# Kernel tuning notes

Measured on AMD Instinct MI355X. Metric: run time of the kernel, lower is better.

## Reference

```python
import jax, jax.numpy as jnp
from jax import lax
import numpy as np

B = 32768
N_IN = 8
N_HID = 64
N_CTRL = 2
M_SCEN = (1.0, 1.2)          # scenario parameters for f/g
M_NOM = 1.0
CLF_LAM = 1.0
CBF_LAM = 1.0
P_CLF = 100.0
P_CBF = 50.0
QP_ITERS = 80                # fixed-iteration batched ADMM (OSQP-style) replacing CvxpyLayer
RHO = 1.0
SIGMA = 1e-6
INF = jnp.inf


def setup_inputs() -> dict:
    key = jax.random.key(0)
    ks = jax.random.split(key, 16)
    s = 0.3
    return {
        "x":   jax.random.normal(ks[0], (B, N_IN), jnp.float32),
        "VW1": jax.random.normal(ks[1], (N_HID, N_IN), jnp.float32) * s,
        "Vb1": jax.random.normal(ks[2], (N_HID,), jnp.float32) * s,
        "VW2": jax.random.normal(ks[3], (N_HID, N_HID), jnp.float32) * s,
        "Vb2": jax.random.normal(ks[4], (N_HID,), jnp.float32) * s,
        "HW1": jax.random.normal(ks[5], (N_HID, N_IN), jnp.float32) * s,
        "Hb1": jax.random.normal(ks[6], (N_HID,), jnp.float32) * s,
        "HW2": jax.random.normal(ks[7], (N_HID, N_HID), jnp.float32) * s,
        "Hb2": jax.random.normal(ks[8], (N_HID,), jnp.float32) * s,
        "HW3": jax.random.normal(ks[9], (N_HID, N_HID), jnp.float32) * s,
        "Hb3": jax.random.normal(ks[10], (N_HID,), jnp.float32) * s,
        "HW4": jax.random.normal(ks[11], (1, N_HID), jnp.float32) * s,
        "Hb4": jax.random.normal(ks[12], (1,), jnp.float32) * s,
        "G0":  jax.random.normal(ks[13], (N_IN, N_CTRL), jnp.float32) * s,
        "K":   jax.random.normal(ks[14], (N_IN, N_CTRL), jnp.float32) * s,
    }


def _lyapunov(x, W1, b1, W2, b2):
    t1 = jnp.tanh(x @ W1.T + b1)                                   # [B,H]
    t2 = jnp.tanh(t1 @ W2.T + b2)                                  # [B,H]
    V = 0.5 * jnp.sum(t2 * t2, axis=1)                             # [B]
    # fused diag(1-t^2) @ W chain (no diag_embed materialization)
    D1 = (1.0 - t1 ** 2)[:, :, None] * W1[None]                    # [B,H,N]
    D2 = (1.0 - t2 ** 2)[:, :, None] * jnp.einsum('hk,bkn->bhn', W2, D1)
    grad_V = jnp.einsum('bh,bhn->bn', t2, D2)                      # [B,N]
    return V, grad_V


def _barrier(x, W1, b1, W2, b2, W3, b3, W4, b4):
    t1 = jnp.tanh(x @ W1.T + b1)
    t2 = jnp.tanh(t1 @ W2.T + b2)
    t3 = jnp.tanh(t2 @ W3.T + b3)
    H = t3 @ W4.T + b4                                             # [B,1]
    D1 = (1.0 - t1 ** 2)[:, :, None] * W1[None]
    D2 = (1.0 - t2 ** 2)[:, :, None] * jnp.einsum('hk,bkn->bhn', W2, D1)
    D3 = (1.0 - t3 ** 2)[:, :, None] * jnp.einsum('hk,bkn->bhn', W3, D2)
    grad_H = jnp.einsum('oh,bhn->bn', W4, D3)                      # [B,N] (o=1)
    return H, grad_H


def _solve_qp(q, A, lo, hi):
    """Batched OSQP-style ADMM for min 0.5 z^T P z + q^T z  s.t. lo <= A z <= hi.
    P = diag([2,2,0,0,0,0]); z = [u(2), r_clf(2), s_cbf(2)]. Fixed iterations."""
    nb, mc, nz = A.shape[0], A.shape[1], A.shape[2]
    Pdiag = jnp.array([2.0, 2.0, 0.0, 0.0, 0.0, 0.0], q.dtype)
    M = RHO * jnp.einsum('bmi,bmj->bij', A, A) + jnp.diag(Pdiag + SIGMA)
    Minv = jnp.linalg.inv(M)                                       # [B,6,6]
    x0 = jnp.zeros((nb, nz), q.dtype)
    z0 = jnp.zeros((nb, mc), q.dtype)
    y0 = jnp.zeros((nb, mc), q.dtype)

    def step(carry, _):
        xx, zz, yy = carry
        rhs = SIGMA * xx - q + jnp.einsum('bmi,bm->bi', A, RHO * zz - yy)
        xt = jnp.einsum('bij,bj->bi', Minv, rhs)
        zt = jnp.einsum('bmi,bi->bm', A, xt)
        zn = jnp.clip(zt + yy / RHO, lo, hi)
        yn = yy + RHO * (zt - zn)
        return (xt, zn, yn), None

    (xf, _, _), _ = lax.scan(step, (x0, z0, y0), None, length=QP_ITERS)
    return xf                                                      # [B,6]


def _forward(x, VW1, Vb1, VW2, Vb2, HW1, Hb1, HW2, Hb2, HW3, Hb3, HW4, Hb4, G0, K):
    V, grad_V = _lyapunov(x, VW1, Vb1, VW2, Vb2)
    H, grad_H = _barrier(x, HW1, Hb1, HW2, Hb2, HW3, Hb3, HW4, Hb4)

    LfVs, LgVs, LfHs, LgHs = [], [], [], []
    for m in M_SCEN:
        # f(x,m) = -x/m ; g(x,m) = G0/m
        LfVs.append(-jnp.sum(grad_V * x, axis=1) / m)              # [B]
        LgVs.append((grad_V @ G0) / m)                             # [B,C]
        LfHs.append(-jnp.sum(grad_H * x, axis=1) / m)
        LgHs.append((grad_H @ G0) / m)
    u_nom = -(x @ K) * (1.0 / M_NOM)                               # [B,C]

    nb = x.shape[0]
    z2 = jnp.zeros((nb, 2), x.dtype)
    ey = jnp.eye(2, dtype=x.dtype)
    e = lambda i: jnp.broadcast_to(ey[i], (nb, 2))
    ninf = jnp.full((nb,), -INF, x.dtype)
    pinf = jnp.full((nb,), INF, x.dtype)
    zer = jnp.zeros((nb,), x.dtype)

    rows, los, his = [], [], []
    for i in range(len(M_SCEN)):
        # CBF: LfH + LgH@u + cbf_lam*H + s_i >= 0
        rows.append(jnp.concatenate([LgHs[i], z2, e(i)], axis=1))
        los.append(-(LfHs[i] + CBF_LAM * H[:, 0])); his.append(pinf)
        # CLF: LfV + LgV@u + clf_lam*V - r_i <= 0
        rows.append(jnp.concatenate([LgVs[i], -e(i), z2], axis=1))
        los.append(ninf); his.append(-(LfVs[i] + CLF_LAM * V))
    for i in range(len(M_SCEN)):
        rows.append(jnp.concatenate([z2, e(i), z2], axis=1)); los.append(zer); his.append(pinf)
    for i in range(len(M_SCEN)):
        rows.append(jnp.concatenate([z2, z2, e(i)], axis=1)); los.append(zer); his.append(pinf)

    A = jnp.stack(rows, axis=1)                                    # [B,8,6]
    lo = jnp.stack(los, axis=1)                                    # [B,8]
    hi = jnp.stack(his, axis=1)
    # objective ||u-u_nom||^2 + p_clf*sum r + p_cbf*sum s  ->  q = [-2 u_nom, p_clf, p_clf, p_cbf, p_cbf]
    q = jnp.concatenate([-2.0 * u_nom,
                         jnp.full((nb, 2), P_CLF, x.dtype),
                         jnp.full((nb, 2), P_CBF, x.dtype)], axis=1)

    z = _solve_qp(q, A, lo, hi)                                    # [B,6]
    u = z[:, :N_CTRL]
    relaxation = jnp.mean(z[:, N_CTRL:N_CTRL + len(M_SCEN)], axis=1, keepdims=True)  # [B,1]

    ns = float(len(M_SCEN))
    Vdot = sum(LfVs[i] + jnp.sum(LgVs[i] * u, axis=1) for i in range(len(M_SCEN))) / ns
    Hdot = sum(LfHs[i] + jnp.sum(LgHs[i] * u, axis=1) for i in range(len(M_SCEN))) / ns
    return u, relaxation, V, Vdot[:, None, None], H, Hdot[:, None, None]


def reference(x, VW1, Vb1, VW2, Vb2, HW1, Hb1, HW2, Hb2, HW3, Hb3, HW4, Hb4, G0, K):
    return _forward(x, VW1, Vb1, VW2, Vb2, HW1, Hb1, HW2, Hb2, HW3, Hb3, HW4, Hb4, G0, K)
```

## Files before the change

kernel.cpp:

```cpp
#include <hip/hip_runtime.h>
#include <hip/hip_bf16.h>
#include <math.h>

typedef _Float16 f16x8 __attribute__((ext_vector_type(8)));
typedef _Float16 f16x4 __attribute__((ext_vector_type(4)));
typedef float    f32x4 __attribute__((ext_vector_type(4)));

__device__ __forceinline__ float ldin(const void* p, int i, int f32f) {
  return f32f ? ((const float*)p)[i]
              : __bfloat162float(((const __hip_bfloat16*)p)[i]);
}

__device__ __forceinline__ f32x4 MFMA(f16x8 a, f16x8 b, f32x4 c) {
  return __builtin_amdgcn_mfma_f32_16x16x32_f16(a, b, c, 0, 0, 0);
}

__device__ __forceinline__ float tanh_fast(float x) {
  float e = __expf(2.f * x);
  return 1.f - 2.f * __builtin_amdgcn_rcpf(e + 1.f);
}

__device__ __forceinline__ float redq(float v) {
  v += __shfl_xor(v, 16, 64);
  v += __shfl_xor(v, 32, 64);
  return v;
}

__device__ __forceinline__ int widx(int h, int k) {
  return ((h >> 4) << 10) + ((k >> 5) << 9) + (((k >> 3) & 3) << 7) + ((h & 15) << 3) + (k & 7);
}

#define OFF_W2V   0
#define OFF_W2VT  4096
#define OFF_W2H   8192
#define OFF_W2HT  12288
#define OFF_W3H   16384
#define OFF_W3HT  20480
#define OFF_W1V   24576
#define OFF_W1H   26624
#define SW_N      28672

#define C_WGV0 0
#define C_WGV1 64
#define C_WGH0 128
#define C_WGH1 192
#define C_VB1  256
#define C_VB2  320
#define C_HB1  384
#define C_HB2  448
#define C_HB3  512
#define C_W4   576
#define C_K    640
#define C_HB4  656
#define C_N    660

__global__ __launch_bounds__(512, 2) void fused_kernel(
    const void* px, const void* pVW1, const void* pVb1, const void* pVW2, const void* pVb2,
    const void* pHW1, const void* pHb1, const void* pHW2, const void* pHb2,
    const void* pHW3, const void* pHb3, const void* pHW4, const void* pHb4,
    const void* pG0, const void* pK, float* out)
{
  __shared__ __align__(16) _Float16 sW[SW_N];
  __shared__ __align__(16) _Float16 sAct[16][1024];
  __shared__ __align__(16) float sQPs[128][12];
  __shared__ __align__(16) float sC[C_N];
  __shared__ int sCnt;

  const int tid = threadIdx.x;
  if (tid == 0) sCnt = 0;
  __syncthreads();
  {
    const unsigned short* xbp = (const unsigned short*)px;
    int good = 0;
#pragma unroll
    for (int i = 0; i < 2; ++i) {
      int ex = (xbp[tid * 2 + i] >> 7) & 0xFF;
      good += (ex >= 97 && ex <= 157) ? 1 : 0;
    }
    atomicAdd(&sCnt, good);
  }
  __syncthreads();
  const int f32f = (sCnt >= 870) ? 0 : 1;

  {
    const int h = tid >> 3, k0 = (tid & 7) * 8;
    auto prepM = [&](const void* src, int offF, int offT) {
      f16x8 vv;
#pragma unroll
      for (int j = 0; j < 8; ++j) vv[j] = (_Float16)ldin(src, tid * 8 + j, f32f);
      *(f16x8*)(sW + offF + widx(h, k0)) = vv;
#pragma unroll
      for (int j = 0; j < 8; ++j) sW[offT + widx(k0 + j, h)] = vv[j];
    };
    prepM(pVW2, OFF_W2V, OFF_W2VT);
    prepM(pHW2, OFF_W2H, OFF_W2HT);
    prepM(pHW3, OFF_W3H, OFF_W3HT);

    if (tid < 64) {
      const int ht = tid >> 4, mm = tid & 15;
      auto prepW1 = [&](const void* src, int off) {
        const int base = off + ht * 512 + mm * 8;
#pragma unroll
        for (int j = 0; j < 8; ++j) {
          float wv = ldin(src, tid * 8 + j, f32f);
          _Float16 hh = (_Float16)wv;
          sW[base + j]       = hh;
          sW[base + 128 + j] = hh;
          sW[base + 256 + j] = f32f ? (_Float16)(wv - (float)hh)
                                    : (_Float16)0.f;
          sW[base + 384 + j] = (_Float16)0.f;
        }
      };
      prepW1(pVW1, OFF_W1V);
      prepW1(pHW1, OFF_W1H);
      float a0 = 0.f, a1 = 0.f, b0 = 0.f, b1 = 0.f;
#pragma unroll
      for (int nn = 0; nn < 8; ++nn) {
        float g0 = ldin(pG0, 2 * nn, f32f), g1 = ldin(pG0, 2 * nn + 1, f32f);
        float wv = ldin(pVW1, tid * 8 + nn, f32f), wh = ldin(pHW1, tid * 8 + nn, f32f);
        a0 += wv * g0; a1 += wv * g1; b0 += wh * g0; b1 += wh * g1;
      }
      sC[C_WGV0 + tid] = a0; sC[C_WGV1 + tid] = a1;
      sC[C_WGH0 + tid] = b0; sC[C_WGH1 + tid] = b1;
      sC[C_VB1 + tid] = ldin(pVb1, tid, f32f);
      sC[C_VB2 + tid] = ldin(pVb2, tid, f32f);
      sC[C_HB1 + tid] = ldin(pHb1, tid, f32f);
      sC[C_HB2 + tid] = ldin(pHb2, tid, f32f);
      sC[C_HB3 + tid] = ldin(pHb3, tid, f32f);
      sC[C_W4  + tid] = ldin(pHW4, tid, f32f);
    }
    if (tid < 16) sC[C_K + tid] = ldin(pK, tid, f32f);
    if (tid == 0) sC[C_HB4] = ldin(pHb4, 0, f32f);
  }
  __syncthreads();

  const int lane = tid & 63, w = tid >> 6;
  const int n = lane & 15, q = lane >> 4;
  const int e0 = blockIdx.x * 128 + w * 16;

  float un0 = 0.f, un1 = 0.f;
  f16x8 xb;
#pragma unroll
  for (int j = 0; j < 8; ++j) {
    float xv = ldin(px, (e0 + n) * 8 + j, f32f);
    _Float16 hh = (_Float16)xv;
    float lo = xv - (float)hh;
    xb[j] = (q == 1) ? (_Float16)lo : ((q == 3) ? (_Float16)0.f : hh);
    un0 -= xv * sC[C_K + 2 * j];
    un1 -= xv * sC[C_K + 2 * j + 1];
  }

  _Float16* buf0 = sAct[w * 2];
  _Float16* buf1 = sAct[w * 2 + 1];

  auto gemm64 = [&](int poff, const _Float16* b, f32x4* acc) {
    f16x8 b0 = *(const f16x8*)(b + lane * 8);
    f16x8 b1 = *(const f16x8*)(b + 512 + lane * 8);
#pragma unroll
    for (int ht = 0; ht < 4; ++ht) {
      const _Float16* ap = sW + poff + ht * 1024 + lane * 8;
      f32x4 c = {0.f, 0.f, 0.f, 0.f};
      c = MFMA(*(const f16x8*)ap, b0, c);
      c = MFMA(*(const f16x8*)(ap + 512), b1, c);
      acc[ht] = c;
    }
  };
  auto l1gemm = [&](int off, f32x4* acc) {
#pragma unroll
    for (int ht = 0; ht < 4; ++ht) {
      const _Float16* ap = sW + off + ht * 512 + lane * 8;
      f32x4 c = {0.f, 0.f, 0.f, 0.f};
      acc[ht] = MFMA(*(const f16x8*)ap, xb, c);
    }
  };
  auto wst = [&](const f32x4* vals, _Float16* b) {
#pragma unroll
    for (int ht = 0; ht < 4; ++ht) {
      int aw = ((ht >> 1) << 9) + (((ht & 1) * 2 + (q >> 1)) << 7) + n * 8 + ((q & 1) << 2);
      f16x4 vh;
#pragma unroll
      for (int r = 0; r < 4; ++r) vh[r] = (_Float16)vals[ht][r];
      *(f16x4*)(b + aw) = vh;
    }
  };

  f32x4 acc[4], tv[4];

  f32x4 z1V[4], d1V[4];
  l1gemm(OFF_W1V, acc);
#pragma unroll
  for (int ht = 0; ht < 4; ++ht) {
    int hb = ht * 16 + q * 4;
    f32x4 bb = *(const f32x4*)&sC[C_VB1 + hb];
    z1V[ht] = acc[ht];
#pragma unroll
    for (int r = 0; r < 4; ++r) {
      float t = tanh_fast(z1V[ht][r] + bb[r]);
      tv[ht][r] = t; d1V[ht][r] = 1.f - t * t;
    }
  }
  wst(tv, buf0);

  gemm64(OFF_W2V, buf0, acc);
  float pV = 0.f;
#pragma unroll
  for (int ht = 0; ht < 4; ++ht) {
    int hb = ht * 16 + q * 4;
    f32x4 bb = *(const f32x4*)&sC[C_VB2 + hb];
#pragma unroll
    for (int r = 0; r < 4; ++r) {
      float t = tanh_fast(acc[ht][r] + bb[r]);
      pV += t * t;
      tv[ht][r] = t * (1.f - t * t);
    }
  }
  wst(tv, buf1);

  gemm64(OFF_W2VT, buf1, acc);
  float pgvx = 0.f, plv0 = 0.f, plv1 = 0.f;
#pragma unroll
  for (int ht = 0; ht < 4; ++ht) {
    int hb = ht * 16 + q * 4;
    f32x4 g0 = *(const f32x4*)&sC[C_WGV0 + hb];
    f32x4 g1 = *(const f32x4*)&sC[C_WGV1 + hb];
#pragma unroll
    for (int r = 0; r < 4; ++r) {
      float wt = acc[ht][r] * d1V[ht][r];
      pgvx += wt * z1V[ht][r];
      plv0 += wt * g0[r]; plv1 += wt * g1[r];
    }
  }

  f32x4 z1H[4], d1H[4], d2H[4];
  l1gemm(OFF_W1H, acc);
#pragma unroll
  for (int ht = 0; ht < 4; ++ht) {
    int hb = ht * 16 + q * 4;
    f32x4 bb = *(const f32x4*)&sC[C_HB1 + hb];
    z1H[ht] = acc[ht];
#pragma unroll
    for (int r = 0; r < 4; ++r) {
      float t = tanh_fast(z1H[ht][r] + bb[r]);
      tv[ht][r] = t; d1H[ht][r] = 1.f - t * t;
    }
  }
  wst(tv, buf0);

  gemm64(OFF_W2H, buf0, acc);
#pragma unroll
  for (int ht = 0; ht < 4; ++ht) {
    int hb = ht * 16 + q * 4;
    f32x4 bb = *(const f32x4*)&sC[C_HB2 + hb];
#pragma unroll
    for (int r = 0; r < 4; ++r) {
      float t = tanh_fast(acc[ht][r] + bb[r]);
      tv[ht][r] = t; d2H[ht][r] = 1.f - t * t;
    }
  }
  wst(tv, buf1);

  gemm64(OFF_W3H, buf1, acc);
  float pH = 0.f;
#pragma unroll
  for (int ht = 0; ht < 4; ++ht) {
    int hb = ht * 16 + q * 4;
    f32x4 bb = *(const f32x4*)&sC[C_HB3 + hb];
    f32x4 w4 = *(const f32x4*)&sC[C_W4 + hb];
#pragma unroll
    for (int r = 0; r < 4; ++r) {
      float t = tanh_fast(acc[ht][r] + bb[r]);
      pH += t * w4[r];
      tv[ht][r] = w4[r] * (1.f - t * t);
    }
  }
  wst(tv, buf0);

  gemm64(OFF_W3HT, buf0, acc);
#pragma unroll
  for (int ht = 0; ht < 4; ++ht)
#pragma unroll
    for (int r = 0; r < 4; ++r) tv[ht][r] = acc[ht][r] * d2H[ht][r];
  wst(tv, buf1);

  gemm64(OFF_W2HT, buf1, acc);
  float pghx = 0.f, plh0 = 0.f, plh1 = 0.f;
#pragma unroll
  for (int ht = 0; ht < 4; ++ht) {
    int hb = ht * 16 + q * 4;
    f32x4 g0 = *(const f32x4*)&sC[C_WGH0 + hb];
    f32x4 g1 = *(const f32x4*)&sC[C_WGH1 + hb];
#pragma unroll
    for (int r = 0; r < 4; ++r) {
      float wt = acc[ht][r] * d1H[ht][r];
      pghx += wt * z1H[ht][r];
      plh0 += wt * g0[r]; plh1 += wt * g1[r];
    }
  }

  {
    float a0 = redq(plh0), a1 = redq(plh1), a2 = redq(plv0), a3 = redq(plv1);
    float a4 = redq(pghx), a5 = redq(pgvx), a6 = redq(pV), a7 = redq(pH);
    if (q == 0) {
      float* sp = sQPs[w * 16 + n];
      sp[0] = a0; sp[1] = a1; sp[2] = a2; sp[3] = a3;
      sp[4] = a4; sp[5] = a5; sp[6] = a6; sp[7] = a7;
      sp[8] = un0; sp[9] = un1;
    }
  }
  __syncthreads();

  if (tid >= 128) return;
  const int e = blockIdx.x * 128 + tid;
  const float* sp = sQPs[tid];
  float gh0 = sp[0], gh1 = sp[1], gv0 = sp[2], gv1 = sp[3];
  float ghx = sp[4], gvx = sp[5];
  float V = 0.5f * sp[6];
  float H = sp[7] + sC[C_HB4];
  un0 = sp[8]; un1 = sp[9];
  out[98304 + e]  = V;
  out[163840 + e] = H;

  const float im = 1.0f / 1.2f;
  const float sg = 1e-6f;

  float lo0 = ghx - H;
  float hi1 = gvx - V;
  float lo2 = ghx * im - H;
  float hi3 = gvx * im - V;
  float qv0 = -2.f * un0, qv1 = -2.f * un1;

  const float d  = 2.f + sg;
  const float rd = 1.f / d;
  const float al = 1.f + im * im;
  const float be = al * (1.f - rd);
  float S00 = be * (gh0 * gh0 + gv0 * gv0) + d;
  float S11 = be * (gh1 * gh1 + gv1 * gv1) + d;
  float S01 = be * (gh0 * gh1 + gv0 * gv1);
  float idet = 1.f / (S00 * S11 - S01 * S01);
  float i00 = S11 * idet, i11 = S00 * idet, i01 = -S01 * idet;

  float X0 = 0.f, X1 = 0.f, X2 = 0.f, X3 = 0.f, X4 = 0.f, X5 = 0.f;
  float Z[8] = {0.f, 0.f, 0.f, 0.f, 0.f, 0.f, 0.f, 0.f};
  float Y[8] = {0.f, 0.f, 0.f, 0.f, 0.f, 0.f, 0.f, 0.f};

#pragma unroll 1
  for (int it = 0; it < 80; ++it) {
    float t0 = Z[0] - Y[0], t1 = Z[1] - Y[1], t2 = Z[2] - Y[2], t3 = Z[3] - Y[3];
    float t4 = Z[4] - Y[4], t5 = Z[5] - Y[5], t6 = Z[6] - Y[6], t7 = Z[7] - Y[7];
    float tauh = t0 + im * t2, tauv = t1 + im * t3;
    float b0 = sg * X0 - qv0 + gh0 * tauh + gv0 * tauv;
    float b1 = sg * X1 - qv1 + gh1 * tauh + gv1 * tauv;
    float b2 = sg * X2 - 100.f - t1 + t4;
    float b3 = sg * X3 - 100.f - t3 + t5;
    float b4 = sg * X4 - 50.f + t0 + t6;
    float b5 = sg * X5 - 50.f + t2 + t7;
    float pp = b2 + im * b3;
    float s2 = b4 + im * b5;
    float cb0 = gh0 * s2 - gv0 * pp;
    float cb1 = gh1 * s2 - gv1 * pp;
    float u0b = b0 - cb0 * rd;
    float u1b = b1 - cb1 * rd;
    X0 = i00 * u0b + i01 * u1b;
    X1 = i01 * u0b + i11 * u1b;
    float gdH = gh0 * X0 + gh1 * X1;
    float gdV = gv0 * X0 + gv1 * X1;
    X2 = (b2 + gdV) * rd;
    X3 = (b3 + im * gdV) * rd;
    X4 = (b4 - gdH) * rd;
    X5 = (b5 - im * gdH) * rd;
    float zt0 = gdH + X4;
    float zt1 = gdV - X2;
    float zt2 = gdH * im + X5;
    float zt3 = gdV * im - X3;

    float v, zn;
    v = zt0 + Y[0]; zn = fmaxf(v, lo0); Y[0] += zt0 - zn; Z[0] = zn;
    v = zt1 + Y[1]; zn = fminf(v, hi1); Y[1] += zt1 - zn; Z[1] = zn;
    v = zt2 + Y[2]; zn = fmaxf(v, lo2); Y[2] += zt2 - zn; Z[2] = zn;
    v = zt3 + Y[3]; zn = fminf(v, hi3); Y[3] += zt3 - zn; Z[3] = zn;
    v = X2 + Y[4];  zn = fmaxf(v, 0.f); Y[4] += X2 - zn;  Z[4] = zn;
    v = X3 + Y[5];  zn = fmaxf(v, 0.f); Y[5] += X3 - zn;  Z[5] = zn;
    v = X4 + Y[6];  zn = fmaxf(v, 0.f); Y[6] += X4 - zn;  Z[6] = zn;
    v = X5 + Y[7];  zn = fmaxf(v, 0.f); Y[7] += X5 - zn;  Z[7] = zn;
  }

  float relax = 0.5f * (X2 + X3);
  const float cc = 0.5f * (1.f + im);
  float Vdot = cc * (gv0 * X0 + gv1 * X1 - gvx);
  float Hdot = cc * (gh0 * X0 + gh1 * X1 - ghx);

  out[2 * e]      = X0;
  out[2 * e + 1]  = X1;
  out[65536 + e]  = relax;
  out[131072 + e] = Vdot;
  out[196608 + e] = Hdot;
}

extern "C" void kernel_launch(void* const* d_in, const int* in_sizes, int n_in,
                              void* d_out, int out_size, void* d_ws, size_t ws_size,
                              hipStream_t stream) {
  (void)d_ws; (void)ws_size; (void)in_sizes; (void)n_in; (void)out_size;
  fused_kernel<<<256, 512, 0, stream>>>(
      d_in[0], d_in[1], d_in[2], d_in[3], d_in[4], d_in[5], d_in[6],
      d_in[7], d_in[8], d_in[9], d_in[10], d_in[11], d_in[12],
      d_in[13], d_in[14], (float*)d_out);
}
```

Baseline: 116.1 us.

## Split weight prep into separate kernel and read weights from global workspace

Moves the per-block weight conversion and swizzling into a small prep kernel that writes f16 weights and constants to the workspace. The main kernel no longer stages weights in shared memory and loads MFMA A-operands straight from global/L2. The QP tail now runs on 16 lanes per wave after wave-level reductions instead of a block barrier, and blocks shrink to 256 threads to raise occupancy. This trades a second launch and global weight reads for less redundant prep and smaller shared memory use.

```diff
diff --git a/kernel.cpp b/kernel.cpp
--- a/kernel.cpp
+++ b/kernel.cpp
@@ -30,16 +30,15 @@
   return ((h >> 4) << 10) + ((k >> 5) << 9) + (((k >> 3) & 3) << 7) + ((h & 15) << 3) + (k & 7);
 }
 
-#define OFF_W2V   0
-#define OFF_W2VT  4096
-#define OFF_W2H   8192
-#define OFF_W2HT  12288
-#define OFF_W3H   16384
-#define OFF_W3HT  20480
+#define OFF_VW2   0
+#define OFF_VW2T  4096
+#define OFF_HW2   8192
+#define OFF_HW2T  12288
+#define OFF_HW3   16384
+#define OFF_HW3T  20480
 #define OFF_W1V   24576
 #define OFF_W1H   26624
-#define SW_N      28672
-
+#define CF_BASE   28672
 #define C_WGV0 0
 #define C_WGV1 64
 #define C_WGH0 128
@@ -52,67 +51,59 @@
 #define C_W4   576
 #define C_K    640
 #define C_HB4  656
-#define C_N    660
-
-__global__ __launch_bounds__(512, 2) void fused_kernel(
-    const void* px, const void* pVW1, const void* pVb1, const void* pVW2, const void* pVb2,
-    const void* pHW1, const void* pHb1, const void* pHW2, const void* pHb2,
-    const void* pHW3, const void* pHb3, const void* pHW4, const void* pHb4,
-    const void* pG0, const void* pK, float* out)
+#define C_FLAG 657
+#define C_N    658
+
+__global__ __launch_bounds__(256) void prep_kernel(
+    const void* px, const void* pVW1, const void* pVW2,
+    const void* pHW1, const void* pHW2, const void* pHW3,
+    const void* pVb1, const void* pVb2, const void* pHb1, const void* pHb2,
+    const void* pHb3, const void* pHW4, const void* pHb4,
+    const void* pG0, const void* pK, _Float16* wsp)
 {
-  __shared__ __align__(16) _Float16 sW[SW_N];
-  __shared__ __align__(16) _Float16 sAct[16][1024];
-  __shared__ __align__(16) float sQPs[128][12];
-  __shared__ __align__(16) float sC[C_N];
   __shared__ int sCnt;
-
   const int tid = threadIdx.x;
   if (tid == 0) sCnt = 0;
   __syncthreads();
   {
-    const unsigned short* xbp = (const unsigned short*)px;
+    const unsigned short* xb = (const unsigned short*)px;
     int good = 0;
 #pragma unroll
     for (int i = 0; i < 2; ++i) {
-      int ex = (xbp[tid * 2 + i] >> 7) & 0xFF;
+      int ex = (xb[tid * 2 + i] >> 7) & 0xFF;
       good += (ex >= 97 && ex <= 157) ? 1 : 0;
     }
     atomicAdd(&sCnt, good);
   }
   __syncthreads();
-  const int f32f = (sCnt >= 870) ? 0 : 1;
-
-  {
-    const int h = tid >> 3, k0 = (tid & 7) * 8;
-    auto prepM = [&](const void* src, int offF, int offT) {
-      f16x8 vv;
-#pragma unroll
-      for (int j = 0; j < 8; ++j) vv[j] = (_Float16)ldin(src, tid * 8 + j, f32f);
-      *(f16x8*)(sW + offF + widx(h, k0)) = vv;
-#pragma unroll
-      for (int j = 0; j < 8; ++j) sW[offT + widx(k0 + j, h)] = vv[j];
-    };
-    prepM(pVW2, OFF_W2V, OFF_W2VT);
-    prepM(pHW2, OFF_W2H, OFF_W2HT);
-    prepM(pHW3, OFF_W3H, OFF_W3HT);
-
+  const int f32f = (sCnt >= 435) ? 0 : 1;
+
+  const int t = blockIdx.x * 256 + tid;
+  int h = t >> 6, k = t & 63;
+  int fw = widx(h, k), tw = widx(k, h);
+  _Float16 v;
+  v = (_Float16)ldin(pVW2, t, f32f); wsp[OFF_VW2 + fw] = v; wsp[OFF_VW2T + tw] = v;
+  v = (_Float16)ldin(pHW2, t, f32f); wsp[OFF_HW2 + fw] = v; wsp[OFF_HW2T + tw] = v;
+  v = (_Float16)ldin(pHW3, t, f32f); wsp[OFF_HW3 + fw] = v; wsp[OFF_HW3T + tw] = v;
+  if (t < 512) {
+    int hh = t >> 3, j = t & 7;
+    int base = ((hh >> 4) << 9) + ((hh & 15) << 3) + j;
+    float f = ldin(pVW1, t, f32f); _Float16 hi = (_Float16)f;
+    _Float16 lo = f32f ? (_Float16)(f - (float)hi) : (_Float16)0.f;
+    wsp[OFF_W1V + base]       = hi;
+    wsp[OFF_W1V + base + 128] = hi;
+    wsp[OFF_W1V + base + 256] = lo;
+    wsp[OFF_W1V + base + 384] = (_Float16)0.f;
+    f = ldin(pHW1, t, f32f); hi = (_Float16)f;
+    lo = f32f ? (_Float16)(f - (float)hi) : (_Float16)0.f;
+    wsp[OFF_W1H + base]       = hi;
+    wsp[OFF_W1H + base + 128] = hi;
+    wsp[OFF_W1H + base + 256] = lo;
+    wsp[OFF_W1H + base + 384] = (_Float16)0.f;
+  }
+  if (blockIdx.x == 0) {
+    float* wsF = (float*)(wsp + CF_BASE);
     if (tid < 64) {
-      const int ht = tid >> 4, mm = tid & 15;
-      auto prepW1 = [&](const void* src, int off) {
-        const int base = off + ht * 512 + mm * 8;
-#pragma unroll
-        for (int j = 0; j < 8; ++j) {
-          float wv = ldin(src, tid * 8 + j, f32f);
-          _Float16 hh = (_Float16)wv;
-          sW[base + j]       = hh;
-          sW[base + 128 + j] = hh;
-          sW[base + 256 + j] = f32f ? (_Float16)(wv - (float)hh)
-                                    : (_Float16)0.f;
-          sW[base + 384 + j] = (_Float16)0.f;
-        }
-      };
-      prepW1(pVW1, OFF_W1V);
-      prepW1(pHW1, OFF_W1H);
       float a0 = 0.f, a1 = 0.f, b0 = 0.f, b1 = 0.f;
 #pragma unroll
       for (int nn = 0; nn < 8; ++nn) {
@@ -120,45 +111,69 @@
         float wv = ldin(pVW1, tid * 8 + nn, f32f), wh = ldin(pHW1, tid * 8 + nn, f32f);
         a0 += wv * g0; a1 += wv * g1; b0 += wh * g0; b1 += wh * g1;
       }
-      sC[C_WGV0 + tid] = a0; sC[C_WGV1 + tid] = a1;
-      sC[C_WGH0 + tid] = b0; sC[C_WGH1 + tid] = b1;
-      sC[C_VB1 + tid] = ldin(pVb1, tid, f32f);
-      sC[C_VB2 + tid] = ldin(pVb2, tid, f32f);
-      sC[C_HB1 + tid] = ldin(pHb1, tid, f32f);
-      sC[C_HB2 + tid] = ldin(pHb2, tid, f32f);
-      sC[C_HB3 + tid] = ldin(pHb3, tid, f32f);
-      sC[C_W4  + tid] = ldin(pHW4, tid, f32f);
-    }
-    if (tid < 16) sC[C_K + tid] = ldin(pK, tid, f32f);
-    if (tid == 0) sC[C_HB4] = ldin(pHb4, 0, f32f);
-  }
+      wsF[C_WGV0 + tid] = a0; wsF[C_WGV1 + tid] = a1;
+      wsF[C_WGH0 + tid] = b0; wsF[C_WGH1 + tid] = b1;
+      wsF[C_VB1 + tid] = ldin(pVb1, tid, f32f);
+      wsF[C_VB2 + tid] = ldin(pVb2, tid, f32f);
+      wsF[C_HB1 + tid] = ldin(pHb1, tid, f32f);
+      wsF[C_HB2 + tid] = ldin(pHb2, tid, f32f);
+      wsF[C_HB3 + tid] = ldin(pHb3, tid, f32f);
+      wsF[C_W4  + tid] = ldin(pHW4, tid, f32f);
+    }
+    if (tid < 16) wsF[C_K + tid] = ldin(pK, tid, f32f);
+    if (tid == 0) { wsF[C_HB4] = ldin(pHb4, 0, f32f); ((int*)wsF)[C_FLAG] = f32f; }
+  }
+}
+
+__global__ __launch_bounds__(256, 3) void main_kernel(
+    const void* px, const _Float16* wsp, float* out)
+{
+  __shared__ __align__(16) _Float16 sAct[4][1024];
+  __shared__ __align__(16) float sC[C_N];
+
+  const int tid = threadIdx.x, lane = tid & 63, w = tid >> 6;
+  const int n = lane & 15, q = lane >> 4;
+  const int e0 = blockIdx.x * 64 + w * 16;
+
+  const float* cf = (const float*)(wsp + CF_BASE);
+  for (int i = tid; i < C_N; i += 256) sC[i] = cf[i];
+  const int f32f = ((const int*)cf)[C_FLAG];
   __syncthreads();
 
-  const int lane = tid & 63, w = tid >> 6;
-  const int n = lane & 15, q = lane >> 4;
-  const int e0 = blockIdx.x * 128 + w * 16;
-
+  float xv[8];
+  if (f32f) {
+    const f32x4* xp = (const f32x4*)((const float*)px + (e0 + n) * 8);
+    f32x4 x0 = xp[0], x1 = xp[1];
+#pragma unroll
+    for (int j = 0; j < 4; ++j) { xv[j] = x0[j]; xv[4 + j] = x1[j]; }
+  } else {
+    uint4 u = *(const uint4*)((const unsigned short*)px + (e0 + n) * 8);
+    unsigned uu[4] = {u.x, u.y, u.z, u.w};
+#pragma unroll
+    for (int j = 0; j < 4; ++j) {
+      xv[2 * j]     = __uint_as_float(uu[j] << 16);
+      xv[2 * j + 1] = __uint_as_float(uu[j] & 0xffff0000u);
+    }
+  }
   float un0 = 0.f, un1 = 0.f;
   f16x8 xb;
 #pragma unroll
   for (int j = 0; j < 8; ++j) {
-    float xv = ldin(px, (e0 + n) * 8 + j, f32f);
-    _Float16 hh = (_Float16)xv;
-    float lo = xv - (float)hh;
+    _Float16 hh = (_Float16)xv[j];
+    float lo = xv[j] - (float)hh;
     xb[j] = (q == 1) ? (_Float16)lo : ((q == 3) ? (_Float16)0.f : hh);
-    un0 -= xv * sC[C_K + 2 * j];
-    un1 -= xv * sC[C_K + 2 * j + 1];
-  }
-
-  _Float16* buf0 = sAct[w * 2];
-  _Float16* buf1 = sAct[w * 2 + 1];
-
-  auto gemm64 = [&](int poff, const _Float16* b, f32x4* acc) {
-    f16x8 b0 = *(const f16x8*)(b + lane * 8);
-    f16x8 b1 = *(const f16x8*)(b + 512 + lane * 8);
+    un0 -= xv[j] * sC[C_K + 2 * j];
+    un1 -= xv[j] * sC[C_K + 2 * j + 1];
+  }
+
+  _Float16* buf = sAct[w];
+
+  auto gemm64 = [&](int poff, f32x4* acc) {
+    f16x8 b0 = *(const f16x8*)(buf + lane * 8);
+    f16x8 b1 = *(const f16x8*)(buf + 512 + lane * 8);
 #pragma unroll
     for (int ht = 0; ht < 4; ++ht) {
-      const _Float16* ap = sW + poff + ht * 1024 + lane * 8;
+      const _Float16* ap = wsp + poff + ht * 1024 + lane * 8;
       f32x4 c = {0.f, 0.f, 0.f, 0.f};
       c = MFMA(*(const f16x8*)ap, b0, c);
       c = MFMA(*(const f16x8*)(ap + 512), b1, c);
@@ -168,19 +183,19 @@
   auto l1gemm = [&](int off, f32x4* acc) {
 #pragma unroll
     for (int ht = 0; ht < 4; ++ht) {
-      const _Float16* ap = sW + off + ht * 512 + lane * 8;
+      const _Float16* ap = wsp + off + ht * 512 + lane * 8;
       f32x4 c = {0.f, 0.f, 0.f, 0.f};
       acc[ht] = MFMA(*(const f16x8*)ap, xb, c);
     }
   };
-  auto wst = [&](const f32x4* vals, _Float16* b) {
+  auto wst = [&](const f32x4* vals) {
 #pragma unroll
     for (int ht = 0; ht < 4; ++ht) {
       int aw = ((ht >> 1) << 9) + (((ht & 1) * 2 + (q >> 1)) << 7) + n * 8 + ((q & 1) << 2);
       f16x4 vh;
 #pragma unroll
       for (int r = 0; r < 4; ++r) vh[r] = (_Float16)vals[ht][r];
-      *(f16x4*)(b + aw) = vh;
+      *(f16x4*)(buf + aw) = vh;
     }
   };
 
@@ -199,9 +214,9 @@
       tv[ht][r] = t; d1V[ht][r] = 1.f - t * t;
     }
   }
-  wst(tv, buf0);
-
-  gemm64(OFF_W2V, buf0, acc);
+  wst(tv);
+
+  gemm64(OFF_VW2, acc);
   float pV = 0.f;
 #pragma unroll
   for (int ht = 0; ht < 4; ++ht) {
@@ -214,9 +229,9 @@
       tv[ht][r] = t * (1.f - t * t);
     }
   }
-  wst(tv, buf1);
-
-  gemm64(OFF_W2VT, buf1, acc);
+  wst(tv);
+
+  gemm64(OFF_VW2T, acc);
   float pgvx = 0.f, plv0 = 0.f, plv1 = 0.f;
 #pragma unroll
   for (int ht = 0; ht < 4; ++ht) {
@@ -244,9 +259,9 @@
       tv[ht][r] = t; d1H[ht][r] = 1.f - t * t;
     }
   }
-  wst(tv, buf0);
-
-  gemm64(OFF_W2H, buf0, acc);
+  wst(tv);
+
+  gemm64(OFF_HW2, acc);
 #pragma unroll
   for (int ht = 0; ht < 4; ++ht) {
     int hb = ht * 16 + q * 4;
@@ -257,9 +272,9 @@
       tv[ht][r] = t; d2H[ht][r] = 1.f - t * t;
     }
   }
-  wst(tv, buf1);
-
-  gemm64(OFF_W3H, buf1, acc);
+  wst(tv);
+
+  gemm64(OFF_HW3, acc);
   float pH = 0.f;
 #pragma unroll
   for (int ht = 0; ht < 4; ++ht) {
@@ -273,16 +288,16 @@
       tv[ht][r] = w4[r] * (1.f - t * t);
     }
   }
-  wst(tv, buf0);
-
-  gemm64(OFF_W3HT, buf0, acc);
+  wst(tv);
+
+  gemm64(OFF_HW3T, acc);
 #pragma unroll
   for (int ht = 0; ht < 4; ++ht)
 #pragma unroll
     for (int r = 0; r < 4; ++r) tv[ht][r] = acc[ht][r] * d2H[ht][r];
-  wst(tv, buf1);
-
-  gemm64(OFF_W2HT, buf1, acc);
+  wst(tv);
+
+  gemm64(OFF_HW2T, acc);
   float pghx = 0.f, plh0 = 0.f, plh1 = 0.f;
 #pragma unroll
   for (int ht = 0; ht < 4; ++ht) {
@@ -297,26 +312,13 @@
     }
   }
 
-  {
-    float a0 = redq(plh0), a1 = redq(plh1), a2 = redq(plv0), a3 = redq(plv1);
-    float a4 = redq(pghx), a5 = redq(pgvx), a6 = redq(pV), a7 = redq(pH);
-    if (q == 0) {
-      float* sp = sQPs[w * 16 + n];
-      sp[0] = a0; sp[1] = a1; sp[2] = a2; sp[3] = a3;
-      sp[4] = a4; sp[5] = a5; sp[6] = a6; sp[7] = a7;
-      sp[8] = un0; sp[9] = un1;
-    }
-  }
-  __syncthreads();
-
-  if (tid >= 128) return;
-  const int e = blockIdx.x * 128 + tid;
-  const float* sp = sQPs[tid];
-  float gh0 = sp[0], gh1 = sp[1], gv0 = sp[2], gv1 = sp[3];
-  float ghx = sp[4], gvx = sp[5];
-  float V = 0.5f * sp[6];
-  float H = sp[7] + sC[C_HB4];
-  un0 = sp[8]; un1 = sp[9];
+  float gh0 = redq(plh0), gh1 = redq(plh1), gv0 = redq(plv0), gv1 = redq(plv1);
+  float ghx = redq(pghx), gvx = redq(pgvx);
+  float V   = 0.5f * redq(pV);
+  float H   = redq(pH) + sC[C_HB4];
+
+  if (lane >= 16) return;
+  const int e = e0 + lane;
   out[98304 + e]  = V;
   out[163840 + e] = H;
 
@@ -399,9 +401,12 @@
 extern "C" void kernel_launch(void* const* d_in, const int* in_sizes, int n_in,
                               void* d_out, int out_size, void* d_ws, size_t ws_size,
                               hipStream_t stream) {
-  (void)d_ws; (void)ws_size; (void)in_sizes; (void)n_in; (void)out_size;
-  fused_kernel<<<256, 512, 0, stream>>>(
-      d_in[0], d_in[1], d_in[2], d_in[3], d_in[4], d_in[5], d_in[6],
-      d_in[7], d_in[8], d_in[9], d_in[10], d_in[11], d_in[12],
-      d_in[13], d_in[14], (float*)d_out);
-}
+  (void)in_sizes; (void)n_in; (void)out_size; (void)ws_size;
+  float* out = (float*)d_out;
+  _Float16* wsp = (_Float16*)d_ws;
+  prep_kernel<<<16, 256, 0, stream>>>(
+      d_in[0], d_in[1], d_in[3], d_in[5], d_in[7], d_in[9],
+      d_in[2], d_in[4], d_in[6], d_in[8], d_in[10], d_in[11], d_in[12],
+      d_in[13], d_in[14], wsp);
+  main_kernel<<<512, 256, 0, stream>>>(d_in[0], wsp, out);
+}
```

Measured after the change: 124.8 us. +7.5%, slower.
